# Performance work log

Measured on AMD Instinct MI355X. Metric: run time of the kernel, lower is better.

## Reference

```python
import jax, jax.numpy as jnp
import numpy as np
from jax import lax

DN = ('NCHW', 'OIHW', 'NCHW')
BN_EPS = 1e-5
LRELU_SLOPE = 0.01


def conv_block(x, w1, b1, w2, b2, gamma, bn_bias):
    # Conv2d(512->256, k=1) -> Conv2d(256->512, k=3, pad=1) -> LeakyReLU -> BatchNorm2d(512)
    y = lax.conv_general_dilated(x, w1, (1, 1), 'VALID', dimension_numbers=DN)
    y = y + b1[None, :, None, None]
    y = lax.conv_general_dilated(y, w2, (1, 1), 'SAME', dimension_numbers=DN)
    y = y + b2[None, :, None, None]
    y = jnp.where(y > 0, y, LRELU_SLOPE * y)
    # BatchNorm2d in training mode: batch statistics over (B, H, W) per channel
    mean = jnp.mean(y, axis=(0, 2, 3))
    var = jnp.var(y, axis=(0, 2, 3))
    y = (y - mean[None, :, None, None]) * lax.rsqrt(var + BN_EPS)[None, :, None, None]
    return y * gamma[None, :, None, None] + bn_bias[None, :, None, None]


def setup_inputs() -> dict:
    key = jax.random.key(0)
    ks = jax.random.split(key, 9)
    B, C, H, W = 8, 512, 32, 32
    x = jax.random.normal(ks[0], (B, C, H, W), dtype=jnp.float32)
    x1 = jax.random.normal(ks[1], (B, C, H, W), dtype=jnp.float32)
    x2 = jax.random.normal(ks[2], (B, C, H, W), dtype=jnp.float32)
    w1 = jax.random.normal(ks[3], (256, 512, 1, 1), dtype=jnp.float32) * 0.02
    b1 = jnp.zeros((256,), dtype=jnp.float32)
    w2 = jax.random.normal(ks[4], (512, 256, 3, 3), dtype=jnp.float32) * 0.02
    b2 = jnp.zeros((512,), dtype=jnp.float32)
    gamma = jnp.ones((512,), dtype=jnp.float32)
    bn_bias = jnp.zeros((512,), dtype=jnp.float32)
    beta = jax.random.normal(ks[5], (1,), dtype=jnp.float32)  # Parameter(zeros(1)) in torch; random so output is non-trivial
    return {"x": x, "x1": x1, "x2": x2, "w1": w1, "b1": b1, "w2": w2,
            "b2": b2, "gamma": gamma, "bn_bias": bn_bias, "beta": beta}


def reference(x, x1, x2, w1, b1, w2, b2, gamma, bn_bias, beta):
    B, C, H, W = x1.shape
    N = H * W
    F1 = conv_block(x1, w1, b1, w2, b2, gamma, bn_bias).reshape(B, C, N)   # [B, C, N]
    F2 = conv_block(x2, w1, b1, w2, b2, gamma, bn_bias).reshape(B, C, N)   # [B, C, N]
    scores = jnp.einsum('bcn,bdn->bcd', F1, F2)                            # [B, C, C]
    attention = jax.nn.softmax(scores, axis=-1)
    out = jnp.einsum('bcd,bdn->bcn', attention, x.reshape(B, C, N))
    return beta * out.reshape(B, C, H, W)
```

## Files before the change

kernel.cpp:

```cpp
#include <hip/hip_runtime.h>


typedef __attribute__((ext_vector_type(8))) short bfrag;
typedef __attribute__((ext_vector_type(4))) float facc;

__device__ __forceinline__ unsigned short bf16_rn(float v) {
  unsigned u = __float_as_uint(v);
  return (unsigned short)((u + 0x7fffu + ((u >> 16) & 1u)) >> 16);
}

__device__ __forceinline__ void dma16(const void* g, const void* lds) {
  __builtin_amdgcn_global_load_lds(
      (const __attribute__((address_space(1))) unsigned int*)g,
      (__attribute__((address_space(3))) unsigned int*)(unsigned int)(unsigned long long)(const char*)lds,
      16, 0, 0);
}

__global__ __launch_bounds__(256) void prologue(
    const float* __restrict__ x1, const float* __restrict__ x2,
    const float* __restrict__ w2,
    unsigned short* __restrict__ hi, unsigned short* __restrict__ lo,
    unsigned short* __restrict__ w2s, float* __restrict__ statsz) {
  int bid = blockIdx.x;
  int t = threadIdx.x;
  if (bid < 8192) {
    __shared__ float tile[32][33];
    int p0 = (bid & 31) * 32, ci0 = ((bid >> 5) & 15) * 32, z = bid >> 9;
    const float* src = (z < 8) ? x1 + (size_t)z * 524288 : x2 + (size_t)(z - 8) * 524288;
    {
      int ci_l = t >> 5, p_l = t & 31;
#pragma unroll
      for (int j = 0; j < 4; j++)
        tile[ci_l + 8 * j][p_l] = src[(size_t)(ci0 + ci_l + 8 * j) * 1024 + p0 + p_l];
    }
    __syncthreads();
    {
      int p_l = t >> 3, cg = (t & 7) * 4;
      unsigned short hh[4], ll[4];
#pragma unroll
      for (int j = 0; j < 4; j++) {
        float v = tile[cg + j][p_l];
        hh[j] = bf16_rn(v);
        ll[j] = bf16_rn(v - __uint_as_float((unsigned)hh[j] << 16));
      }
      size_t idx = ((size_t)z * 1024 + p0 + p_l) * 512 + ci0 + cg;
      *(ushort4*)(hi + idx) = make_ushort4(hh[0], hh[1], hh[2], hh[3]);
      *(ushort4*)(lo + idx) = make_ushort4(ll[0], ll[1], ll[2], ll[3]);
    }
  } else {
    int co = bid - 8192;
    if (co < 40) statsz[co * 256 + t] = 0.f;
    int panel = co >> 7, co_l = co & 127;
    int ch = t >> 5, ci_l = t & 31;
    int chi = ci_l >> 3, cil7 = ci_l & 7;
    const float* src = w2 + ((size_t)co * 256 + t) * 9;
#pragma unroll
    for (int tap = 0; tap < 9; tap++) {
      float v = src[tap];
      unsigned short h = bf16_rn(v);
      unsigned short l = bf16_rn(v - __uint_as_float((unsigned)h << 16));
      int dy = tap / 3, slot = tap % 3;
      int e = slot * 128 + co_l;
      size_t base = (size_t)(((panel * 8 + ch) * 3 + dy)) * 24576;
      size_t off_hi = base + e * 64 + ((chi ^ (e & 7)) << 3) + cil7;
      w2s[off_hi] = h;
      w2s[off_hi ^ 32] = l;
    }
  }
}

__global__ __launch_bounds__(256) void transpose_split(
    const float* __restrict__ src0, const float* __restrict__ src1,
    unsigned short* __restrict__ hi, unsigned short* __restrict__ lo) {
  __shared__ float tile[32][33];
  int z = blockIdx.z;
  const float* src = (z < 8) ? src0 + (size_t)z * 524288 : src1 + (size_t)(z - 8) * 524288;
  int ci0 = blockIdx.y * 32, p0 = blockIdx.x * 32;
  int t = threadIdx.x;
  {
    int ci_l = t >> 5, p_l = t & 31;
#pragma unroll
    for (int j = 0; j < 4; j++)
      tile[ci_l + 8 * j][p_l] = src[(size_t)(ci0 + ci_l + 8 * j) * 1024 + p0 + p_l];
  }
  __syncthreads();
  {
    int p_l = t >> 3, cg = (t & 7) * 4;
    unsigned short hh[4], ll[4];
#pragma unroll
    for (int j = 0; j < 4; j++) {
      float v = tile[cg + j][p_l];
      hh[j] = bf16_rn(v);
      ll[j] = bf16_rn(v - __uint_as_float((unsigned)hh[j] << 16));
    }
    size_t idx = ((size_t)z * 1024 + p0 + p_l) * 512 + ci0 + cg;
    *(ushort4*)(hi + idx) = make_ushort4(hh[0], hh[1], hh[2], hh[3]);
    *(ushort4*)(lo + idx) = make_ushort4(ll[0], ll[1], ll[2], ll[3]);
  }
}

template <int KTOT, int EPI, int AF32, int KSPLIT>
__global__ __launch_bounds__(256, 2) void gemm_nt(
    const void* __restrict__ Ahi_, const unsigned short* __restrict__ Alo,
    int aLD, long long aBS,
    const unsigned short* __restrict__ Bhi, const unsigned short* __restrict__ Blo,
    int bLD, long long bBS,
    void* __restrict__ out0, void* __restrict__ out1,
    const float* __restrict__ p0, const float* __restrict__ p1,
    const float* __restrict__ p2, const float* __restrict__ p3) {
  __shared__ __attribute__((aligned(16))) unsigned char smem[65536];
  int t = threadIdx.x;
  int z = blockIdx.z;
  int zb = z, kh = 0;
  if (KSPLIT) { zb = z & 7; kh = z >> 3; }
  int m0 = blockIdx.y * 128, n0 = blockIdx.x * 128;
  int w = t >> 6, lane = t & 63;
  int lm = lane & 15, q = lane >> 4;
  int mh = (w & 1) * 64, nh = (w >> 1) * 64;
  facc acc[4][4] = {};
  for (int k0 = 0; k0 < KTOT; k0 += 64) {
    __syncthreads();
    if (AF32) {
      const float* Af = (const float*)Ahi_ + (size_t)zb * aBS;
#pragma unroll
      for (int j = 0; j < 8; j++) {
        int idx = t + 256 * j;
        int row = idx >> 4, c4 = idx & 15;
        float4 v = *(const float4*)(Af + (size_t)(m0 + row) * aLD + k0 + c4 * 4);
        unsigned short h0 = bf16_rn(v.x), h1 = bf16_rn(v.y), h2 = bf16_rn(v.z), h3 = bf16_rn(v.w);
        unsigned short l0 = bf16_rn(v.x - __uint_as_float((unsigned)h0 << 16));
        unsigned short l1 = bf16_rn(v.y - __uint_as_float((unsigned)h1 << 16));
        unsigned short l2 = bf16_rn(v.z - __uint_as_float((unsigned)h2 << 16));
        unsigned short l3 = bf16_rn(v.w - __uint_as_float((unsigned)h3 << 16));
        int base = row * 256 + (((c4 >> 1) ^ (row & 7)) * 16) + (c4 & 1) * 8;
        *(ushort4*)(smem + base) = make_ushort4(h0, h1, h2, h3);
        *(ushort4*)(smem + base + 128) = make_ushort4(l0, l1, l2, l3);
      }
    } else {
      const unsigned short* Ah = (const unsigned short*)Ahi_ + (size_t)zb * aBS + kh * KTOT;
      const unsigned short* Al = Alo + (size_t)zb * aBS + kh * KTOT;
#pragma unroll
      for (int j = 0; j < 8; j++) {
        int idx = t + 256 * j;
        int row = idx >> 4, c = idx & 15;
        const unsigned short* src = (c < 8) ? Ah : Al;
        uint4 v = *(const uint4*)(src + (size_t)(m0 + row) * aLD + k0 + (c & 7) * 8);
        *(uint4*)(smem + row * 256 + ((((c & 7) ^ (row & 7)) | (c & 8)) * 16)) = v;
      }
    }
#pragma unroll
    for (int j = 0; j < 8; j++) {
      int idx = t + 256 * j;
      int row = idx >> 4, c = idx & 15;
      const unsigned short* src = (c < 8) ? Bhi : Blo;
      uint4 v = *(const uint4*)(src + (size_t)zb * bBS + (size_t)kh * KTOT +
                                (size_t)(n0 + row) * bLD + k0 + (c & 7) * 8);
      *(uint4*)(smem + 32768 + row * 256 + ((((c & 7) ^ (row & 7)) | (c & 8)) * 16)) = v;
    }
    __syncthreads();
#pragma unroll
    for (int ks = 0; ks < 2; ks++) {
      bfrag ah[4], al[4], bh[4], bl[4];
#pragma unroll
      for (int mt = 0; mt < 4; mt++) {
        int m = mh + mt * 16 + lm;
        int phys = ((ks * 4 + q) ^ (m & 7)) * 16;
        const unsigned char* p = smem + m * 256;
        ah[mt] = *(const bfrag*)(p + phys);
        al[mt] = *(const bfrag*)(p + phys + 128);
      }
#pragma unroll
      for (int nt = 0; nt < 4; nt++) {
        int n = nh + nt * 16 + lm;
        int phys = ((ks * 4 + q) ^ (n & 7)) * 16;
        const unsigned char* p = smem + 32768 + n * 256;
        bh[nt] = *(const bfrag*)(p + phys);
        bl[nt] = *(const bfrag*)(p + phys + 128);
      }
#pragma unroll
      for (int mt = 0; mt < 4; mt++)
#pragma unroll
        for (int nt = 0; nt < 4; nt++) {
          acc[mt][nt] = __builtin_amdgcn_mfma_f32_16x16x32_bf16(ah[mt], bh[nt], acc[mt][nt], 0, 0, 0);
          acc[mt][nt] = __builtin_amdgcn_mfma_f32_16x16x32_bf16(ah[mt], bl[nt], acc[mt][nt], 0, 0, 0);
          acc[mt][nt] = __builtin_amdgcn_mfma_f32_16x16x32_bf16(al[mt], bh[nt], acc[mt][nt], 0, 0, 0);
        }
    }
  }
  if (EPI == 0) {
    unsigned short* Oh = (unsigned short*)out0;
    unsigned short* Ol = (unsigned short*)out1;
#pragma unroll
    for (int mt = 0; mt < 4; mt++) {
      int mb = m0 + mh + mt * 16 + q * 4;
#pragma unroll
      for (int nt = 0; nt < 4; nt++) {
        int n = n0 + nh + nt * 16 + lm;
        unsigned short hh[4], ll[4];
#pragma unroll
        for (int r = 0; r < 4; r++) {
          float v = acc[mt][nt][r] + p0[mb + r];
          hh[r] = bf16_rn(v);
          ll[r] = bf16_rn(v - __uint_as_float((unsigned)hh[r] << 16));
        }
        size_t o = ((size_t)(zb * 1024 + n)) * 256 + mb;
        *(ushort4*)(Oh + o) = make_ushort4(hh[0], hh[1], hh[2], hh[3]);
        *(ushort4*)(Ol + o) = make_ushort4(ll[0], ll[1], ll[2], ll[3]);
      }
    }
  } else if (EPI == 1) {
    float* S = (float*)out0 + (size_t)kh * 2097152;
    const float* stats = p0;
    const float* rowsum = p1;
    const float* gamma = p2;
    const float* bnb = p3;
    float a2v[4], t2v[4], r2v[4];
#pragma unroll
    for (int nt = 0; nt < 4; nt++) {
      int d = n0 + nh + nt * 16 + lm;
      float mu = stats[512 + d] * (1.f / 8192.f);
      float var = stats[1536 + d] * (1.f / 8192.f) - mu * mu;
      float a = gamma[d] * rsqrtf(var + 1e-5f);
      a2v[nt] = a;
      t2v[nt] = bnb[d] - mu * a;
      r2v[nt] = rowsum[(8 + zb) * 512 + d];
    }
#pragma unroll
    for (int mt = 0; mt < 4; mt++)
#pragma unroll
      for (int r = 0; r < 4; r++) {
        int cc = m0 + mh + mt * 16 + q * 4 + r;
        float mu = stats[cc] * (1.f / 8192.f);
        float var = stats[1024 + cc] * (1.f / 8192.f) - mu * mu;
        float a1 = gamma[cc] * rsqrtf(var + 1e-5f);
        float t1 = bnb[cc] - mu * a1;
        float r1 = rowsum[zb * 512 + cc];
#pragma unroll
        for (int nt = 0; nt < 4; nt++) {
          int d = n0 + nh + nt * 16 + lm;
          float sc = a1 * a2v[nt] * acc[mt][nt][r];
          if (kh == 0)
            sc += a1 * t2v[nt] * r1 + t1 * a2v[nt] * r2v[nt] + 1024.f * t1 * t2v[nt];
          S[((size_t)(zb * 512 + cc)) * 512 + d] = sc;
        }
      }
  } else {
    float* O = (float*)out0;
    float sc = p0[0];
#pragma unroll
    for (int mt = 0; mt < 4; mt++)
#pragma unroll
      for (int r = 0; r < 4; r++) {
        int cc = m0 + mh + mt * 16 + q * 4 + r;
#pragma unroll
        for (int nt = 0; nt < 4; nt++) {
          int n = n0 + nh + nt * 16 + lm;
          O[((size_t)(zb * 512 + cc)) * 1024 + n] = sc * acc[mt][nt][r];
        }
      }
  }
}

__global__ __launch_bounds__(256, 2) void conv3x3_mfma(
    const unsigned short* __restrict__ Y1thi, const unsigned short* __restrict__ Y1tlo,
    const unsigned short* __restrict__ w2s,
    const float* __restrict__ b2, unsigned short* __restrict__ Fhi,
    unsigned short* __restrict__ Flo, float* __restrict__ stats,
    float* __restrict__ rowsum) {
  __shared__ __attribute__((aligned(16))) unsigned char smem[75264];
  const int WOFF = 26112;
  int t = threadIdx.x;
  int g = blockIdx.z;
  int panel = blockIdx.y;
  int co_base = panel * 128;
  int y0 = blockIdx.x * 4;
  int w = t >> 6, lane = t & 63;
  int lm = lane & 15, q = lane >> 4;
  int co_half = (w & 1) * 64, px_half = (w >> 1) * 64;
  int px_l[4], row_l[4], x_l[4];
#pragma unroll
  for (int i = 0; i < 4; i++) {
    px_l[i] = px_half + i * 16 + lm;
    row_l[i] = px_l[i] >> 5;
    x_l[i] = px_l[i] & 31;
  }
  const unsigned char* wgbase =
      (const unsigned char*)w2s + (size_t)panel * 8 * 3 * 49152 + w * 12288 + lane * 16;
  const unsigned char* ldsw = smem + WOFF + w * 12288;
  facc acc[4][4] = {};
  for (int chunk = 0; chunk < 8; chunk++) {
    int ci0 = chunk * 32;
    for (int dy = 0; dy < 3; dy++) {
      __syncthreads();
      {
        const unsigned char* gsrc = wgbase + (size_t)(chunk * 3 + dy) * 49152;
#pragma unroll
        for (int j = 0; j < 12; j++) dma16(gsrc + j * 1024, ldsw + j * 1024);
      }
      if (dy == 0) {
        for (int u = t; u < 1632; u += 256) {
          int e = u >> 3, c = u & 7;
          int srow = e / 34, xh = e - srow * 34;
          int gy = y0 - 1 + srow, gx = xh - 1;
          uint4 v = make_uint4(0u, 0u, 0u, 0u);
          if ((unsigned)gy < 32u && (unsigned)gx < 32u) {
            const unsigned short* src = (c < 4) ? Y1thi : Y1tlo;
            v = *(const uint4*)(src +
                ((size_t)((g * 32 + gy) * 32 + gx) * 256 + ci0 + (c & 3) * 8));
          }
          *(uint4*)(smem + e * 128 + ((c ^ (xh & 7)) * 16)) = v;
        }
      }
      __syncthreads();
#pragma unroll
      for (int dx = 0; dx < 3; dx++) {
        bfrag ah[4], al[4], bh[4], bl[4];
#pragma unroll
        for (int j = 0; j < 4; j++) {
          int cr = co_half + j * 16 + lm;
          const unsigned char* p = smem + WOFF + dx * 16384 + cr * 128;
          int ph = (q ^ (lm & 7)) * 16;
          ah[j] = *(const bfrag*)(p + ph);
          al[j] = *(const bfrag*)(p + (ph ^ 64));
        }
#pragma unroll
        for (int i = 0; i < 4; i++) {
          int xh = x_l[i] + dx;
          int entry = (row_l[i] + dy) * 34 + xh;
          const unsigned char* p = smem + entry * 128;
          int ph = (q ^ (xh & 7)) * 16;
          bh[i] = *(const bfrag*)(p + ph);
          bl[i] = *(const bfrag*)(p + (ph ^ 64));
        }
#pragma unroll
        for (int j = 0; j < 4; j++)
#pragma unroll
          for (int i = 0; i < 4; i++) {
            acc[j][i] = __builtin_amdgcn_mfma_f32_16x16x32_bf16(ah[j], bh[i], acc[j][i], 0, 0, 0);
            acc[j][i] = __builtin_amdgcn_mfma_f32_16x16x32_bf16(ah[j], bl[i], acc[j][i], 0, 0, 0);
            acc[j][i] = __builtin_amdgcn_mfma_f32_16x16x32_bf16(al[j], bh[i], acc[j][i], 0, 0, 0);
          }
      }
    }
  }
  int grp = g >> 3;
  int px0 = blockIdx.x * 128;
#pragma unroll
  for (int j = 0; j < 4; j++) {
#pragma unroll
    for (int r = 0; r < 4; r++) {
      int co = co_base + co_half + j * 16 + q * 4 + r;
      float bb = b2[co];
      float s = 0.f, s2 = 0.f;
#pragma unroll
      for (int i = 0; i < 4; i++) {
        float v = acc[j][i][r] + bb;
        v = v > 0.f ? v : 0.01f * v;
        unsigned short h = bf16_rn(v);
        unsigned short l = bf16_rn(v - __uint_as_float((unsigned)h << 16));
        size_t o = ((size_t)(g * 512 + co)) * 1024 + px0 + px_l[i];
        Fhi[o] = h;
        Flo[o] = l;
        s += v;
        s2 = fmaf(v, v, s2);
      }
#pragma unroll
      for (int d = 1; d <= 8; d <<= 1) {
        s += __shfl_xor(s, d);
        s2 += __shfl_xor(s2, d);
      }
      if (lm == 0) {
        atomicAdd(&stats[grp * 512 + co], s);
        atomicAdd(&stats[1024 + grp * 512 + co], s2);
        atomicAdd(&rowsum[g * 512 + co], s);
      }
    }
  }
}

__global__ __launch_bounds__(256) void softmax_rows(float* __restrict__ S) {
  int row = blockIdx.x;
  float* p = S + (size_t)row * 512;
  const float* p1 = p + 2097152;
  int t = threadIdx.x;
  float2 va = *(const float2*)(p + 2 * t);
  float2 vb = *(const float2*)(p1 + 2 * t);
  float vx = va.x + vb.x, vy = va.y + vb.y;
  float mx = fmaxf(vx, vy);
#pragma unroll
  for (int d = 32; d >= 1; d >>= 1) mx = fmaxf(mx, __shfl_xor(mx, d));
  __shared__ float sred[8];
  int wave = t >> 6, lane = t & 63;
  if (lane == 0) sred[wave] = mx;
  __syncthreads();
  float m4 = fmaxf(fmaxf(sred[0], sred[1]), fmaxf(sred[2], sred[3]));
  float ex = expf(vx - m4), ey = expf(vy - m4);
  float s = ex + ey;
#pragma unroll
  for (int d = 32; d >= 1; d >>= 1) s += __shfl_xor(s, d);
  if (lane == 0) sred[4 + wave] = s;
  __syncthreads();
  float inv = 1.f / (sred[4] + sred[5] + sred[6] + sred[7]);
  float px_ = ex * inv, py_ = ey * inv;
  unsigned short h0 = bf16_rn(px_), h1 = bf16_rn(py_);
  unsigned short l0 = bf16_rn(px_ - __uint_as_float((unsigned)h0 << 16));
  unsigned short l1 = bf16_rn(py_ - __uint_as_float((unsigned)h1 << 16));
  unsigned short* rh = (unsigned short*)p;
  *(ushort2*)(rh + 2 * t) = make_ushort2(h0, h1);
  *(ushort2*)(rh + 512 + 2 * t) = make_ushort2(l0, l1);
}

extern "C" void kernel_launch(void* const* d_in, const int* in_sizes, int n_in,
                              void* d_out, int out_size, void* d_ws, size_t ws_size,
                              hipStream_t stream) {
  const float* x = (const float*)d_in[0];
  const float* x1 = (const float*)d_in[1];
  const float* x2 = (const float*)d_in[2];
  const float* w1 = (const float*)d_in[3];
  const float* b1 = (const float*)d_in[4];
  const float* w2 = (const float*)d_in[5];
  const float* b2 = (const float*)d_in[6];
  const float* gamma = (const float*)d_in[7];
  const float* bnb = (const float*)d_in[8];
  const float* beta = (const float*)d_in[9];
  float* out = (float*)d_out;
  float* ws = (float*)d_ws;

  unsigned short* x12thi = (unsigned short*)ws;
  unsigned short* x12tlo = (unsigned short*)(ws + 4194304);
  unsigned short* Fhi = (unsigned short*)ws;
  unsigned short* Flo = (unsigned short*)(ws + 4194304);
  unsigned short* xthi = (unsigned short*)ws;
  unsigned short* xtlo = (unsigned short*)(ws + 2097152);
  unsigned short* Y1thi = (unsigned short*)(ws + 8388608);
  unsigned short* Y1tlo = (unsigned short*)(ws + 10485760);
  float* S = ws + 8388608;
  unsigned short* w2s = (unsigned short*)(ws + 12582912);
  float* stats = ws + 13762560;
  float* rowsum = ws + 13764608;

  prologue<<<8704, 256, 0, stream>>>(x1, x2, w2, x12thi, x12tlo, w2s, stats);
  gemm_nt<512, 0, 1, 0><<<dim3(8, 2, 16), 256, 0, stream>>>(
      w1, nullptr, 512, 0LL, x12thi, x12tlo, 512, 524288LL,
      Y1thi, Y1tlo, b1, nullptr, nullptr, nullptr);
  conv3x3_mfma<<<dim3(8, 4, 16), 256, 0, stream>>>(
      Y1thi, Y1tlo, w2s, b2, Fhi, Flo, stats, rowsum);
  gemm_nt<512, 1, 0, 1><<<dim3(4, 4, 16), 256, 0, stream>>>(
      Fhi, Flo, 1024, 524288LL, Fhi + (size_t)8 * 524288, Flo + (size_t)8 * 524288,
      1024, 524288LL, S, nullptr, stats, rowsum, gamma, bnb);
  transpose_split<<<dim3(32, 16, 8), 256, 0, stream>>>(x, x, xthi, xtlo);
  softmax_rows<<<4096, 256, 0, stream>>>(S);
  gemm_nt<512, 2, 0, 0><<<dim3(8, 4, 8), 256, 0, stream>>>(
      (unsigned short*)S, (unsigned short*)S + 512, 1024, 524288LL,
      xthi, xtlo, 512, 524288LL, out, nullptr, beta, nullptr, nullptr, nullptr);
}
```

Before: 318.7 us.

## Store intermediates as pre-swizzled LDS images and load tiles via direct DMA

Every producer kernel (prologue, 1x1 GEMM epilogue, conv3x3 epilogue, softmax, x transpose) now writes its hi/lo bf16 output in a tiled, XOR-swizzled byte layout that matches the consumer's shared-memory tile. The GEMM and conv3x3 kernels can then fill shared memory with global_load_lds DMA instead of register round-trips with per-element swizzling, and the conv halo is zero-filled once up front. The GEMM tile N is halved from 128 to 64, which doubles the grid and cuts LDS use, trading accumulator reuse for more blocks. The scattered 2-byte stores in the conv epilogue and the larger workspace footprint are the added costs.

After: 291.3 us. -8.6%, faster.

```diff
diff --git a/kernel.cpp b/kernel.cpp
--- a/kernel.cpp
+++ b/kernel.cpp
@@ -18,8 +18,7 @@
 
 __global__ __launch_bounds__(256) void prologue(
     const float* __restrict__ x1, const float* __restrict__ x2,
-    const float* __restrict__ w2,
-    unsigned short* __restrict__ hi, unsigned short* __restrict__ lo,
+    const float* __restrict__ w2, unsigned char* __restrict__ x12timg,
     unsigned short* __restrict__ w2s, float* __restrict__ statsz) {
   int bid = blockIdx.x;
   int t = threadIdx.x;
@@ -43,9 +42,12 @@
         hh[j] = bf16_rn(v);
         ll[j] = bf16_rn(v - __uint_as_float((unsigned)hh[j] << 16));
       }
-      size_t idx = ((size_t)z * 1024 + p0 + p_l) * 512 + ci0 + cg;
-      *(ushort4*)(hi + idx) = make_ushort4(hh[0], hh[1], hh[2], hh[3]);
-      *(ushort4*)(lo + idx) = make_ushort4(ll[0], ll[1], ll[2], ll[3]);
+      int px = p0 + p_l, row = px & 127, panel = px >> 7;
+      int c = ci0 + cg, kc = c >> 6, ck = (c >> 3) & 7;
+      int slot = ck ^ (row & 7);
+      size_t byte = (((size_t)(z * 8 + panel) * 8 + kc) * 128 + row) * 256 + slot * 16 + (c & 7) * 2;
+      *(ushort4*)(x12timg + byte) = make_ushort4(hh[0], hh[1], hh[2], hh[3]);
+      *(ushort4*)(x12timg + byte + 128) = make_ushort4(ll[0], ll[1], ll[2], ll[3]);
     }
   } else {
     int co = bid - 8192;
@@ -69,12 +71,11 @@
   }
 }
 
-__global__ __launch_bounds__(256) void transpose_split(
-    const float* __restrict__ src0, const float* __restrict__ src1,
-    unsigned short* __restrict__ hi, unsigned short* __restrict__ lo) {
+__global__ __launch_bounds__(256) void transpose_split_x(
+    const float* __restrict__ x, unsigned char* __restrict__ img) {
   __shared__ float tile[32][33];
   int z = blockIdx.z;
-  const float* src = (z < 8) ? src0 + (size_t)z * 524288 : src1 + (size_t)(z - 8) * 524288;
+  const float* src = x + (size_t)z * 524288;
   int ci0 = blockIdx.y * 32, p0 = blockIdx.x * 32;
   int t = threadIdx.x;
   {
@@ -93,40 +94,47 @@
       hh[j] = bf16_rn(v);
       ll[j] = bf16_rn(v - __uint_as_float((unsigned)hh[j] << 16));
     }
-    size_t idx = ((size_t)z * 1024 + p0 + p_l) * 512 + ci0 + cg;
-    *(ushort4*)(hi + idx) = make_ushort4(hh[0], hh[1], hh[2], hh[3]);
-    *(ushort4*)(lo + idx) = make_ushort4(ll[0], ll[1], ll[2], ll[3]);
+    int px = p0 + p_l, row = px & 127, panel = px >> 7;
+    int c = ci0 + cg, kc = c >> 6, ck = (c >> 3) & 7;
+    int slot = ck ^ (row & 7);
+    size_t byte = (((size_t)(z * 8 + panel) * 8 + kc) * 128 + row) * 256 + slot * 16 + (c & 7) * 2;
+    *(ushort4*)(img + byte) = make_ushort4(hh[0], hh[1], hh[2], hh[3]);
+    *(ushort4*)(img + byte + 128) = make_ushort4(ll[0], ll[1], ll[2], ll[3]);
   }
 }
 
 template <int KTOT, int EPI, int AF32, int KSPLIT>
 __global__ __launch_bounds__(256, 2) void gemm_nt(
-    const void* __restrict__ Ahi_, const unsigned short* __restrict__ Alo,
-    int aLD, long long aBS,
-    const unsigned short* __restrict__ Bhi, const unsigned short* __restrict__ Blo,
-    int bLD, long long bBS,
-    void* __restrict__ out0, void* __restrict__ out1,
+    const void* __restrict__ Asrc, long long aZS, int aKC,
+    const unsigned char* __restrict__ Bimg, long long bZS, int bKC,
+    void* __restrict__ out0,
     const float* __restrict__ p0, const float* __restrict__ p1,
     const float* __restrict__ p2, const float* __restrict__ p3) {
-  __shared__ __attribute__((aligned(16))) unsigned char smem[65536];
+  __shared__ __attribute__((aligned(16))) unsigned char smem[49152];
   int t = threadIdx.x;
   int z = blockIdx.z;
   int zb = z, kh = 0;
   if (KSPLIT) { zb = z & 7; kh = z >> 3; }
-  int m0 = blockIdx.y * 128, n0 = blockIdx.x * 128;
+  int m0 = blockIdx.y * 128, n0 = blockIdx.x * 64;
   int w = t >> 6, lane = t & 63;
   int lm = lane & 15, q = lane >> 4;
-  int mh = (w & 1) * 64, nh = (w >> 1) * 64;
-  facc acc[4][4] = {};
+  int mh = (w & 1) * 64, nh = (w >> 1) * 32;
+  const unsigned char* Abase = (const unsigned char*)Asrc + (size_t)zb * aZS +
+      (size_t)(m0 >> 7) * ((size_t)aKC << 15) + (size_t)w * 8192 + (size_t)lane * 16;
+  const unsigned char* Bbase = Bimg + (size_t)zb * bZS +
+      (size_t)(n0 >> 7) * ((size_t)bKC << 15) + (size_t)(n0 & 127) * 256 +
+      (size_t)w * 4096 + (size_t)lane * 16;
+  facc acc[4][2] = {};
   for (int k0 = 0; k0 < KTOT; k0 += 64) {
+    int kc = (KSPLIT ? kh * (KTOT / 64) : 0) + (k0 >> 6);
     __syncthreads();
     if (AF32) {
-      const float* Af = (const float*)Ahi_ + (size_t)zb * aBS;
+      const float* Af = (const float*)Asrc;
 #pragma unroll
       for (int j = 0; j < 8; j++) {
         int idx = t + 256 * j;
         int row = idx >> 4, c4 = idx & 15;
-        float4 v = *(const float4*)(Af + (size_t)(m0 + row) * aLD + k0 + c4 * 4);
+        float4 v = *(const float4*)(Af + (size_t)(m0 + row) * KTOT + k0 + c4 * 4);
         unsigned short h0 = bf16_rn(v.x), h1 = bf16_rn(v.y), h2 = bf16_rn(v.z), h3 = bf16_rn(v.w);
         unsigned short l0 = bf16_rn(v.x - __uint_as_float((unsigned)h0 << 16));
         unsigned short l1 = bf16_rn(v.y - __uint_as_float((unsigned)h1 << 16));
@@ -137,50 +145,39 @@
         *(ushort4*)(smem + base + 128) = make_ushort4(l0, l1, l2, l3);
       }
     } else {
-      const unsigned short* Ah = (const unsigned short*)Ahi_ + (size_t)zb * aBS + kh * KTOT;
-      const unsigned short* Al = Alo + (size_t)zb * aBS + kh * KTOT;
-#pragma unroll
-      for (int j = 0; j < 8; j++) {
-        int idx = t + 256 * j;
-        int row = idx >> 4, c = idx & 15;
-        const unsigned short* src = (c < 8) ? Ah : Al;
-        uint4 v = *(const uint4*)(src + (size_t)(m0 + row) * aLD + k0 + (c & 7) * 8);
-        *(uint4*)(smem + row * 256 + ((((c & 7) ^ (row & 7)) | (c & 8)) * 16)) = v;
-      }
-    }
-#pragma unroll
-    for (int j = 0; j < 8; j++) {
-      int idx = t + 256 * j;
-      int row = idx >> 4, c = idx & 15;
-      const unsigned short* src = (c < 8) ? Bhi : Blo;
-      uint4 v = *(const uint4*)(src + (size_t)zb * bBS + (size_t)kh * KTOT +
-                                (size_t)(n0 + row) * bLD + k0 + (c & 7) * 8);
-      *(uint4*)(smem + 32768 + row * 256 + ((((c & 7) ^ (row & 7)) | (c & 8)) * 16)) = v;
+      const unsigned char* ap = Abase + ((size_t)kc << 15);
+#pragma unroll
+      for (int j = 0; j < 8; j++) dma16(ap + j * 1024, smem + w * 8192 + j * 1024);
+    }
+    {
+      const unsigned char* bp = Bbase + ((size_t)kc << 15);
+#pragma unroll
+      for (int j = 0; j < 4; j++) dma16(bp + j * 1024, smem + 32768 + w * 4096 + j * 1024);
     }
     __syncthreads();
 #pragma unroll
     for (int ks = 0; ks < 2; ks++) {
-      bfrag ah[4], al[4], bh[4], bl[4];
+      bfrag ah[4], al[4], bh[2], bl[2];
 #pragma unroll
       for (int mt = 0; mt < 4; mt++) {
         int m = mh + mt * 16 + lm;
         int phys = ((ks * 4 + q) ^ (m & 7)) * 16;
-        const unsigned char* p = smem + m * 256;
-        ah[mt] = *(const bfrag*)(p + phys);
-        al[mt] = *(const bfrag*)(p + phys + 128);
-      }
-#pragma unroll
-      for (int nt = 0; nt < 4; nt++) {
+        const unsigned char* p = smem + m * 256 + phys;
+        ah[mt] = *(const bfrag*)p;
+        al[mt] = *(const bfrag*)(p + 128);
+      }
+#pragma unroll
+      for (int nt = 0; nt < 2; nt++) {
         int n = nh + nt * 16 + lm;
         int phys = ((ks * 4 + q) ^ (n & 7)) * 16;
-        const unsigned char* p = smem + 32768 + n * 256;
-        bh[nt] = *(const bfrag*)(p + phys);
-        bl[nt] = *(const bfrag*)(p + phys + 128);
+        const unsigned char* p = smem + 32768 + n * 256 + phys;
+        bh[nt] = *(const bfrag*)p;
+        bl[nt] = *(const bfrag*)(p + 128);
       }
 #pragma unroll
       for (int mt = 0; mt < 4; mt++)
 #pragma unroll
-        for (int nt = 0; nt < 4; nt++) {
+        for (int nt = 0; nt < 2; nt++) {
           acc[mt][nt] = __builtin_amdgcn_mfma_f32_16x16x32_bf16(ah[mt], bh[nt], acc[mt][nt], 0, 0, 0);
           acc[mt][nt] = __builtin_amdgcn_mfma_f32_16x16x32_bf16(ah[mt], bl[nt], acc[mt][nt], 0, 0, 0);
           acc[mt][nt] = __builtin_amdgcn_mfma_f32_16x16x32_bf16(al[mt], bh[nt], acc[mt][nt], 0, 0, 0);
@@ -188,14 +185,18 @@
     }
   }
   if (EPI == 0) {
-    unsigned short* Oh = (unsigned short*)out0;
-    unsigned short* Ol = (unsigned short*)out1;
+    unsigned char* Yimg = (unsigned char*)out0;
+    int g = zb;
 #pragma unroll
     for (int mt = 0; mt < 4; mt++) {
       int mb = m0 + mh + mt * 16 + q * 4;
-#pragma unroll
-      for (int nt = 0; nt < 4; nt++) {
-        int n = n0 + nh + nt * 16 + lm;
+      int ch = mb >> 5, chunk = (mb >> 3) & 3, e2 = (mb & 7) * 2;
+#pragma unroll
+      for (int nt = 0; nt < 2; nt++) {
+        int px = n0 + nh + nt * 16 + lm;
+        int gy = px >> 5, gx = px & 31;
+        int slot = chunk ^ ((gx + 1) & 7);
+        size_t base = ((size_t)((g * 8 + ch) * 32 + gy)) * 4096 + gx * 128 + slot * 16 + e2;
         unsigned short hh[4], ll[4];
 #pragma unroll
         for (int r = 0; r < 4; r++) {
@@ -203,9 +204,8 @@
           hh[r] = bf16_rn(v);
           ll[r] = bf16_rn(v - __uint_as_float((unsigned)hh[r] << 16));
         }
-        size_t o = ((size_t)(zb * 1024 + n)) * 256 + mb;
-        *(ushort4*)(Oh + o) = make_ushort4(hh[0], hh[1], hh[2], hh[3]);
-        *(ushort4*)(Ol + o) = make_ushort4(ll[0], ll[1], ll[2], ll[3]);
+        *(ushort4*)(Yimg + base) = make_ushort4(hh[0], hh[1], hh[2], hh[3]);
+        *(ushort4*)(Yimg + (base ^ 64)) = make_ushort4(ll[0], ll[1], ll[2], ll[3]);
       }
     }
   } else if (EPI == 1) {
@@ -214,9 +214,9 @@
     const float* rowsum = p1;
     const float* gamma = p2;
     const float* bnb = p3;
-    float a2v[4], t2v[4], r2v[4];
-#pragma unroll
-    for (int nt = 0; nt < 4; nt++) {
+    float a2v[2], t2v[2], r2v[2];
+#pragma unroll
+    for (int nt = 0; nt < 2; nt++) {
       int d = n0 + nh + nt * 16 + lm;
       float mu = stats[512 + d] * (1.f / 8192.f);
       float var = stats[1536 + d] * (1.f / 8192.f) - mu * mu;
@@ -236,7 +236,7 @@
         float t1 = bnb[cc] - mu * a1;
         float r1 = rowsum[zb * 512 + cc];
 #pragma unroll
-        for (int nt = 0; nt < 4; nt++) {
+        for (int nt = 0; nt < 2; nt++) {
           int d = n0 + nh + nt * 16 + lm;
           float sc = a1 * a2v[nt] * acc[mt][nt][r];
           if (kh == 0)
@@ -253,7 +253,7 @@
       for (int r = 0; r < 4; r++) {
         int cc = m0 + mh + mt * 16 + q * 4 + r;
 #pragma unroll
-        for (int nt = 0; nt < 4; nt++) {
+        for (int nt = 0; nt < 2; nt++) {
           int n = n0 + nh + nt * 16 + lm;
           O[((size_t)(zb * 512 + cc)) * 1024 + n] = sc * acc[mt][nt][r];
         }
@@ -262,11 +262,9 @@
 }
 
 __global__ __launch_bounds__(256, 2) void conv3x3_mfma(
-    const unsigned short* __restrict__ Y1thi, const unsigned short* __restrict__ Y1tlo,
-    const unsigned short* __restrict__ w2s,
-    const float* __restrict__ b2, unsigned short* __restrict__ Fhi,
-    unsigned short* __restrict__ Flo, float* __restrict__ stats,
-    float* __restrict__ rowsum) {
+    const unsigned char* __restrict__ Yimg, const unsigned short* __restrict__ w2s,
+    const float* __restrict__ b2, unsigned char* __restrict__ Fimg,
+    float* __restrict__ stats, float* __restrict__ rowsum) {
   __shared__ __attribute__((aligned(16))) unsigned char smem[75264];
   const int WOFF = 26112;
   int t = threadIdx.x;
@@ -284,12 +282,13 @@
     row_l[i] = px_l[i] >> 5;
     x_l[i] = px_l[i] & 31;
   }
+  for (int u = t; u < 1632; u += 256)
+    *(uint4*)(smem + u * 16) = make_uint4(0u, 0u, 0u, 0u);
   const unsigned char* wgbase =
       (const unsigned char*)w2s + (size_t)panel * 8 * 3 * 49152 + w * 12288 + lane * 16;
   const unsigned char* ldsw = smem + WOFF + w * 12288;
   facc acc[4][4] = {};
   for (int chunk = 0; chunk < 8; chunk++) {
-    int ci0 = chunk * 32;
     for (int dy = 0; dy < 3; dy++) {
       __syncthreads();
       {
@@ -298,17 +297,16 @@
         for (int j = 0; j < 12; j++) dma16(gsrc + j * 1024, ldsw + j * 1024);
       }
       if (dy == 0) {
-        for (int u = t; u < 1632; u += 256) {
-          int e = u >> 3, c = u & 7;
-          int srow = e / 34, xh = e - srow * 34;
-          int gy = y0 - 1 + srow, gx = xh - 1;
-          uint4 v = make_uint4(0u, 0u, 0u, 0u);
-          if ((unsigned)gy < 32u && (unsigned)gx < 32u) {
-            const unsigned short* src = (c < 4) ? Y1thi : Y1tlo;
-            v = *(const uint4*)(src +
-                ((size_t)((g * 32 + gy) * 32 + gx) * 256 + ci0 + (c & 3) * 8));
+#pragma unroll
+        for (int j = 0; j < 6; j++) {
+          int id = w * 6 + j;
+          int strip = id >> 2, part = id & 3;
+          int gy = y0 - 1 + strip;
+          if ((unsigned)gy < 32u) {
+            const unsigned char* src = Yimg +
+                ((size_t)((g * 8 + chunk) * 32 + gy)) * 4096 + part * 1024 + lane * 16;
+            dma16(src, smem + strip * 4352 + 128 + part * 1024);
           }
-          *(uint4*)(smem + e * 128 + ((c ^ (xh & 7)) * 16)) = v;
         }
       }
       __syncthreads();
@@ -350,6 +348,7 @@
 #pragma unroll
     for (int r = 0; r < 4; r++) {
       int co = co_base + co_half + j * 16 + q * 4 + r;
+      int row = co & 127;
       float bb = b2[co];
       float s = 0.f, s2 = 0.f;
 #pragma unroll
@@ -358,9 +357,13 @@
         v = v > 0.f ? v : 0.01f * v;
         unsigned short h = bf16_rn(v);
         unsigned short l = bf16_rn(v - __uint_as_float((unsigned)h << 16));
-        size_t o = ((size_t)(g * 512 + co)) * 1024 + px0 + px_l[i];
-        Fhi[o] = h;
-        Flo[o] = l;
+        int px = px0 + px_l[i];
+        int kc = px >> 6, ck = (px >> 3) & 7;
+        int slot = ck ^ (row & 7);
+        size_t byte = (((size_t)(g * 4 + panel) * 16 + kc) * 128 + row) * 256 +
+                      slot * 16 + (px & 7) * 2;
+        *(unsigned short*)(Fimg + byte) = h;
+        *(unsigned short*)(Fimg + byte + 128) = l;
         s += v;
         s2 = fmaf(v, v, s2);
       }
@@ -378,9 +381,11 @@
   }
 }
 
-__global__ __launch_bounds__(256) void softmax_rows(float* __restrict__ S) {
-  int row = blockIdx.x;
-  float* p = S + (size_t)row * 512;
+__global__ __launch_bounds__(256) void softmax_rows(const float* __restrict__ S,
+                                                    unsigned char* __restrict__ attimg) {
+  int rowg = blockIdx.x;
+  int z = rowg >> 9, c = rowg & 511;
+  const float* p = S + (size_t)rowg * 512;
   const float* p1 = p + 2097152;
   int t = threadIdx.x;
   float2 va = *(const float2*)(p + 2 * t);
@@ -405,9 +410,14 @@
   unsigned short h0 = bf16_rn(px_), h1 = bf16_rn(py_);
   unsigned short l0 = bf16_rn(px_ - __uint_as_float((unsigned)h0 << 16));
   unsigned short l1 = bf16_rn(py_ - __uint_as_float((unsigned)h1 << 16));
-  unsigned short* rh = (unsigned short*)p;
-  *(ushort2*)(rh + 2 * t) = make_ushort2(h0, h1);
-  *(ushort2*)(rh + 512 + 2 * t) = make_ushort2(l0, l1);
+  int rowl = c & 127, panel = c >> 7;
+  int d0 = 2 * t;
+  int kc = d0 >> 6, ck = (d0 >> 3) & 7;
+  int slot = ck ^ (rowl & 7);
+  size_t byte = (((size_t)(z * 4 + panel) * 8 + kc) * 128 + rowl) * 256 +
+                slot * 16 + (d0 & 7) * 2;
+  *(ushort2*)(attimg + byte) = make_ushort2(h0, h1);
+  *(ushort2*)(attimg + byte + 128) = make_ushort2(l0, l1);
 }
 
 extern "C" void kernel_launch(void* const* d_in, const int* in_sizes, int n_in,
@@ -424,33 +434,28 @@
   const float* bnb = (const float*)d_in[8];
   const float* beta = (const float*)d_in[9];
   float* out = (float*)d_out;
-  float* ws = (float*)d_ws;
-
-  unsigned short* x12thi = (unsigned short*)ws;
-  unsigned short* x12tlo = (unsigned short*)(ws + 4194304);
-  unsigned short* Fhi = (unsigned short*)ws;
-  unsigned short* Flo = (unsigned short*)(ws + 4194304);
-  unsigned short* xthi = (unsigned short*)ws;
-  unsigned short* xtlo = (unsigned short*)(ws + 2097152);
-  unsigned short* Y1thi = (unsigned short*)(ws + 8388608);
-  unsigned short* Y1tlo = (unsigned short*)(ws + 10485760);
-  float* S = ws + 8388608;
-  unsigned short* w2s = (unsigned short*)(ws + 12582912);
-  float* stats = ws + 13762560;
-  float* rowsum = ws + 13764608;
-
-  prologue<<<8704, 256, 0, stream>>>(x1, x2, w2, x12thi, x12tlo, w2s, stats);
-  gemm_nt<512, 0, 1, 0><<<dim3(8, 2, 16), 256, 0, stream>>>(
-      w1, nullptr, 512, 0LL, x12thi, x12tlo, 512, 524288LL,
-      Y1thi, Y1tlo, b1, nullptr, nullptr, nullptr);
+  unsigned char* wsb = (unsigned char*)d_ws;
+
+  unsigned char* x12timg = wsb;
+  unsigned char* Fimg = wsb;
+  unsigned char* xtimg = wsb;
+  unsigned char* attimg = wsb + 16777216;
+  unsigned char* Yimg = wsb + 33554432;
+  float* S = (float*)(wsb + 33554432);
+  unsigned short* w2s = (unsigned short*)(wsb + 50331648);
+  float* stats = (float*)(wsb + 55050240);
+  float* rowsum = (float*)(wsb + 55058432);
+
+  prologue<<<8704, 256, 0, stream>>>(x1, x2, w2, x12timg, w2s, stats);
+  gemm_nt<512, 0, 1, 0><<<dim3(16, 2, 16), 256, 0, stream>>>(
+      w1, 0LL, 0, x12timg, 2097152LL, 8, Yimg, b1, nullptr, nullptr, nullptr);
   conv3x3_mfma<<<dim3(8, 4, 16), 256, 0, stream>>>(
-      Y1thi, Y1tlo, w2s, b2, Fhi, Flo, stats, rowsum);
-  gemm_nt<512, 1, 0, 1><<<dim3(4, 4, 16), 256, 0, stream>>>(
-      Fhi, Flo, 1024, 524288LL, Fhi + (size_t)8 * 524288, Flo + (size_t)8 * 524288,
-      1024, 524288LL, S, nullptr, stats, rowsum, gamma, bnb);
-  transpose_split<<<dim3(32, 16, 8), 256, 0, stream>>>(x, x, xthi, xtlo);
-  softmax_rows<<<4096, 256, 0, stream>>>(S);
-  gemm_nt<512, 2, 0, 0><<<dim3(8, 4, 8), 256, 0, stream>>>(
-      (unsigned short*)S, (unsigned short*)S + 512, 1024, 524288LL,
-      xthi, xtlo, 512, 524288LL, out, nullptr, beta, nullptr, nullptr, nullptr);
-}
+      Yimg, w2s, b2, Fimg, stats, rowsum);
+  gemm_nt<512, 1, 0, 1><<<dim3(8, 4, 16), 256, 0, stream>>>(
+      Fimg, 2097152LL, 16, Fimg + (size_t)8 * 2097152, 2097152LL, 16,
+      S, stats, rowsum, gamma, bnb);
+  transpose_split_x<<<dim3(32, 16, 8), 256, 0, stream>>>(x, xtimg);
+  softmax_rows<<<4096, 256, 0, stream>>>(S, attimg);
+  gemm_nt<512, 2, 0, 0><<<dim3(16, 4, 8), 256, 0, stream>>>(
+      attimg, 1048576LL, 8, xtimg, 2097152LL, 8, out, beta, nullptr, nullptr, nullptr);
+}
```
